# Performance work log

Measured on AMD Instinct MI355X. Metric: run time of the kernel, lower is better.

## Reference

```python
import jax, jax.numpy as jnp
import numpy as np

N_CELL, N_NET, N_GCELL = 50000, 10000, 20000
E = 100000
D = 32   # hidden_node = hidden_net = hidden_hanna = out_node = out_net
DP = 16  # hidden_pin = hidden_edge feats


def setup_inputs() -> dict:
    key = jax.random.key(0)
    ks = jax.random.split(key, 21)
    f = jax.random.normal
    ri = lambda k, n: jax.random.randint(k, (E,), 0, n, dtype=jnp.int32)
    return {
        'node_feat': f(ks[0], (N_CELL, D), jnp.float32),
        'net_feat': f(ks[1], (N_NET, D), jnp.float32),
        'pin_feat': f(ks[2], (E, DP), jnp.float32),
        'hanna_feat': f(ks[3], (N_GCELL, D), jnp.float32),
        'edge_feat': f(ks[4], (E, DP), jnp.float32),
        'pins_src': ri(ks[5], N_CELL), 'pins_dst': ri(ks[6], N_NET),
        'pinned_src': ri(ks[7], N_NET), 'pinned_dst': ri(ks[8], N_CELL),
        'connect_src': ri(ks[9], N_GCELL), 'connect_dst': ri(ks[10], N_GCELL),
        'pt_src': ri(ks[11], N_CELL), 'pt_dst': ri(ks[12], N_GCELL),
        'pf_src': ri(ks[13], N_GCELL), 'pf_dst': ri(ks[14], N_CELL),
        'W_net': f(ks[15], (D, D)) * 0.1, 'b_net': jnp.zeros((D,), jnp.float32),
        'W_topo': f(ks[16], (DP, D * D)) * 0.1, 'b_topo': jnp.zeros((D * D,), jnp.float32),
        'W_pins': f(ks[17], (D, D)) * 0.1, 'b_pins': jnp.zeros((D,), jnp.float32),
        'W_connect': f(ks[18], (D, D)) * 0.1, 'b_connect': jnp.zeros((D,), jnp.float32),
        'W_pt': f(ks[19], (D, D)) * 0.1, 'b_pt': jnp.zeros((D,), jnp.float32),
        'b_pinned': jnp.zeros((D,), jnp.float32), 'b_pf': jnp.zeros((D,), jnp.float32),
    }


def _deg(idx, n):
    # clamped degree, as DGL clamps to min 1
    return jnp.maximum(jax.ops.segment_sum(jnp.ones_like(idx, jnp.float32), idx, n), 1.0)


def graph_conv(h_src, W, b, src, dst, n_src, n_dst):
    # DGL GraphConv with norm='both': D_out^{-1/2} gather -> sum -> D_in^{-1/2}, then W, b
    feat = (h_src * _deg(src, n_src)[:, None] ** -0.5) @ W
    agg = jax.ops.segment_sum(feat[src], dst, n_dst)
    return agg * _deg(dst, n_dst)[:, None] ** -0.5 + b


def nn_conv(h_src, efeat, W_topo, b_topo, bias, src, dst, n_dst):
    # DGL NNConv (aggregator='mean'): per-edge weight from edge_func, mean over in-edges
    d_in = h_src.shape[1]
    w = (efeat @ W_topo + b_topo).reshape(-1, d_in, bias.shape[0])  # (E, d_in, d_out)
    m = jnp.einsum('ei,eio->eo', h_src[src], w)
    return jax.ops.segment_sum(m, dst, n_dst) / _deg(dst, n_dst)[:, None] + bias


def reference(node_feat, net_feat, pin_feat, hanna_feat, edge_feat,
              pins_src, pins_dst, pinned_src, pinned_dst, connect_src, connect_dst,
              pt_src, pt_dst, pf_src, pf_dst,
              W_net, b_net, W_topo, b_topo, W_pins, b_pins,
              W_connect, b_connect, W_pt, b_pt, b_pinned, b_pf):
    # 'pins': cell -> net (GraphConv)
    h_net = graph_conv(node_feat, W_pins, b_pins, pins_src, pins_dst, N_CELL, N_NET)
    # 'pinned': net -> cell (NNConv) + 'point-from': gcell -> cell (NNConv); agg='sum'
    h_cell = (nn_conv(net_feat, pin_feat, W_topo, b_topo, b_pinned, pinned_src, pinned_dst, N_CELL)
              + nn_conv(hanna_feat, edge_feat, W_topo, b_topo, b_pf, pf_src, pf_dst, N_CELL))
    # 'connect': gcell -> gcell + 'point-to': cell -> gcell (GraphConvs); agg='sum'
    h_gcell = (graph_conv(hanna_feat, W_connect, b_connect, connect_src, connect_dst, N_GCELL, N_GCELL)
               + graph_conv(node_feat, W_pt, b_pt, pt_src, pt_dst, N_CELL, N_GCELL))
    return (h_cell, h_net + net_feat @ W_net + b_net, h_gcell)
```

## Files before the change

### kernel.cpp

```cpp
#include <hip/hip_runtime.h>

typedef unsigned short u16;
typedef unsigned int u32;

#define NC 50000
#define NN 10000
#define NG 20000
#define NE 100000
#define NSCAN 150016
#define NBLK 74


__device__ __forceinline__ float bflo(u32 a) { return __uint_as_float(a << 16); }
__device__ __forceinline__ float bfhi(u32 a) { return __uint_as_float(a & 0xFFFF0000u); }
__device__ __forceinline__ u16 fbf(float f) {
  u32 u = __float_as_uint(f);
  return (u16)((u + 0x7FFFu + ((u >> 16) & 1u)) >> 16);
}

__device__ __forceinline__ float nn_msg(int e, int s, const float* __restrict__ ef,
                                        const u16* __restrict__ T,
                                        const float* __restrict__ C, int o) {
  const float4* efp = reinterpret_cast<const float4*>(ef + (size_t)e * 16);
  float4 ea = efp[0], eb = efp[1], ec = efp[2], ed = efp[3];
  const uint4* tp = reinterpret_cast<const uint4*>(T + (size_t)s * 512 + o * 16);
  uint4 ta = tp[0], tb = tp[1];
  float m = C[(size_t)s * 32 + o];
  m += ea.x * bflo(ta.x) + ea.y * bfhi(ta.x) + ea.z * bflo(ta.y) + ea.w * bfhi(ta.y);
  m += eb.x * bflo(ta.z) + eb.y * bfhi(ta.z) + eb.z * bflo(ta.w) + eb.w * bfhi(ta.w);
  m += ec.x * bflo(tb.x) + ec.y * bfhi(tb.x) + ec.z * bflo(tb.y) + ec.w * bfhi(tb.y);
  m += ed.x * bflo(tb.z) + ed.y * bfhi(tb.z) + ed.z * bflo(tb.w) + ed.w * bfhi(tb.w);
  return m;
}

__global__ __launch_bounds__(512, 2) void k_front(
    const float* __restrict__ feat_net, const float* __restrict__ feat_han,
    const float* __restrict__ W_topo, const float* __restrict__ b_topo,
    u16* __restrict__ T_net, u16* __restrict__ T_han,
    float* __restrict__ C_net, float* __restrict__ C_han,
    const int* __restrict__ pins_src, const int* __restrict__ pins_dst,
    const int* __restrict__ pinned_dst, const int* __restrict__ pf_dst,
    const int* __restrict__ connect_src, const int* __restrict__ connect_dst,
    const int* __restrict__ pt_src, const int* __restrict__ pt_dst,
    int* __restrict__ hist, int* __restrict__ srccnt) {
  int b = blockIdx.x;
  int tid = threadIdx.x;
  if (b < 469) {
    __shared__ float hs[64][32];
    int nd0 = b * 64;
    {
      int idx = tid * 4;
      int nl = idx >> 5, i = idx & 31;
      int ng = nd0 + nl;
      int ngc = min(ng, 29999);
      const float* rp = (ngc < NN) ? feat_net + (size_t)ngc * 32
                                   : feat_han + (size_t)(ngc - NN) * 32;
      *reinterpret_cast<float4*>(&hs[nl][i]) =
          *reinterpret_cast<const float4*>(rp + i);
    }
    int j = tid;
    int p = j & 15, o = j >> 4;
    float w[32];
#pragma unroll
    for (int i = 0; i < 32; i++) w[i] = W_topo[p * 1024 + i * 32 + o];
#pragma unroll
    for (int i = 0; i < 32; i++) {
      asm volatile("" : "+v"(w[i]));
    }
    __syncthreads();
#pragma unroll 2
    for (int n = 0; n < 64; n++) {
      const float4* hp = reinterpret_cast<const float4*>(&hs[n][0]);
      float a = 0.f;
#pragma unroll
      for (int q = 0; q < 8; q++) {
        float4 h4 = hp[q];
        a += h4.x * w[4 * q] + h4.y * w[4 * q + 1] +
             h4.z * w[4 * q + 2] + h4.w * w[4 * q + 3];
      }
      int s = nd0 + n;
      if (s < 30000) {
        u16* dst = (s < NN) ? T_net + (size_t)s * 512 + j
                            : T_han + (size_t)(s - NN) * 512 + j;
        *dst = fbf(a);
      }
    }
    return;
  }
  if (b < 2344) {
    int t = (b - 469) * 512 + tid;
    int s2 = t >> 5, o = t & 31;
    bool han = s2 >= NN;
    const float* feat = han ? feat_han : feat_net;
    float* C = han ? C_han : C_net;
    int s = han ? s2 - NN : s2;
    float acc = 0.f;
#pragma unroll 8
    for (int i = 0; i < 32; i++)
      acc += feat[(size_t)s * 32 + i] * b_topo[i * 32 + o];
    C[(size_t)s * 32 + o] = acc;
    return;
  }
  int e = (b - 2344) * 512 + tid;
  if (e >= NE) return;
  atomicAdd(&hist[pins_dst[e]], 1);
  atomicAdd(&hist[10000 + connect_dst[e]], 1);
  atomicAdd(&hist[30000 + pt_dst[e]], 1);
  atomicAdd(&hist[50000 + pinned_dst[e]], 1);
  atomicAdd(&hist[100000 + pf_dst[e]], 1);
  atomicAdd(&srccnt[pins_src[e]], 1);
  atomicAdd(&srccnt[50000 + connect_src[e]], 1);
  atomicAdd(&srccnt[70000 + pt_src[e]], 1);
}

__global__ __launch_bounds__(256) void k_scan1(
    const int* __restrict__ cnt, int* __restrict__ bsum) {
  __shared__ int sm[256];
  int b = blockIdx.x, tid = threadIdx.x;
  int base = b * 2048 + tid * 8;
  int tot = 0;
#pragma unroll
  for (int j = 0; j < 8; j++) {
    int i = base + j;
    tot += (i < NSCAN) ? cnt[i] : 0;
  }
  sm[tid] = tot;
  __syncthreads();
  for (int off = 128; off > 0; off >>= 1) {
    if (tid < off) sm[tid] += sm[tid + off];
    __syncthreads();
  }
  if (tid == 0) bsum[b] = sm[0];
}

__global__ __launch_bounds__(256) void k_scan3(
    const int* __restrict__ cnt, const int* __restrict__ bsum,
    int* __restrict__ bases) {
  __shared__ int sm[256];
  __shared__ int carry;
  int b = blockIdx.x, tid = threadIdx.x;
  if (tid == 0) {
    int run = 0;
    for (int i = 0; i < b; i++) run += bsum[i];
    carry = run;
  }
  int base = b * 2048 + tid * 8;
  int v[8];
  int tot = 0;
#pragma unroll
  for (int j = 0; j < 8; j++) {
    int i = base + j;
    v[j] = (i < NSCAN) ? cnt[i] : 0;
    tot += v[j];
  }
  sm[tid] = tot;
  __syncthreads();
  for (int off = 1; off < 256; off <<= 1) {
    int add = (tid >= off) ? sm[tid - off] : 0;
    __syncthreads();
    sm[tid] += add;
    __syncthreads();
  }
  int excl = sm[tid] - tot + carry;
#pragma unroll
  for (int j = 0; j < 8; j++) {
    int i = base + j;
    if (i < NSCAN) bases[i] = excl;
    excl += v[j];
  }
}

__global__ __launch_bounds__(512) void k_fill(
    const int* __restrict__ pins_src, const int* __restrict__ pins_dst,
    const int* __restrict__ connect_src, const int* __restrict__ connect_dst,
    const int* __restrict__ pt_src, const int* __restrict__ pt_dst,
    const int* __restrict__ pinned_src, const int* __restrict__ pinned_dst,
    const int* __restrict__ pf_src, const int* __restrict__ pf_dst,
    const int* __restrict__ srccnt,
    const int* __restrict__ bases, int* __restrict__ cursor,
    int2* __restrict__ csr_gc, int2* __restrict__ csr_nn) {
  int t = blockIdx.x * 512 + threadIdx.x;
  if (t >= 5 * NE) return;
  int r = (t >= NE) + (t >= 2 * NE) + (t >= 3 * NE) + (t >= 4 * NE);
  int e = t - r * NE;
  const int* srcs = r == 0 ? pins_src : r == 1 ? connect_src
                   : r == 2 ? pt_src : r == 3 ? pinned_src : pf_src;
  const int* dsts = r == 0 ? pins_dst : r == 1 ? connect_dst
                   : r == 2 ? pt_dst : r == 3 ? pinned_dst : pf_dst;
  int off = r == 0 ? 0 : r == 1 ? 10000 : r == 2 ? 30000 : r == 3 ? 50000 : 100000;
  int s = srcs[e];
  int g = off + dsts[e];
  int pos = atomicAdd(&cursor[g], 1);
  int cpos = bases[g] + pos;
  if (r < 3) {
    int soff = r == 0 ? 0 : r == 1 ? 50000 : 70000;
    float w = rsqrtf(fmaxf((float)srccnt[soff + s], 1.f));
    csr_gc[cpos] = make_int2(s, __float_as_int(w));
  } else {
    csr_nn[cpos - 300000] = make_int2(e, s);
  }
}

__global__ __launch_bounds__(512) void k_gc_gather(
    const int* __restrict__ hist, const int* __restrict__ bases,
    const int2* __restrict__ csr_gc,
    const float* __restrict__ node_feat, const float* __restrict__ hanna_feat,
    float* __restrict__ S_net, float* __restrict__ S_conn, float* __restrict__ S_pt) {
  int t = blockIdx.x * 512 + threadIdx.x;
  int rr = t >> 5, o = t & 31;
  int rel = (rr >= 10000) + (rr >= 30000);
  const float* feat = (rel == 1) ? hanna_feat : node_feat;
  float* S = rel == 0 ? S_net + (size_t)rr * 32
           : rel == 1 ? S_conn + (size_t)(rr - 10000) * 32
                      : S_pt + (size_t)(rr - 30000) * 32;
  int base = bases[rr], deg = hist[rr];
  float acc = 0.f;
  int k = 0;
  for (; k + 1 < deg; k += 2) {
    int2 pa = csr_gc[base + k], pb = csr_gc[base + k + 1];
    acc += feat[(size_t)pa.x * 32 + o] * __int_as_float(pa.y) +
           feat[(size_t)pb.x * 32 + o] * __int_as_float(pb.y);
  }
  if (k < deg) {
    int2 pa = csr_gc[base + k];
    acc += feat[(size_t)pa.x * 32 + o] * __int_as_float(pa.y);
  }
  S[o] = acc;
}

__global__ __launch_bounds__(512) void k_tail(
    const int* __restrict__ hist, const int* __restrict__ bases,
    const int2* __restrict__ csr_nn,
    const float* __restrict__ pin_feat, const float* __restrict__ edge_feat,
    const u16* __restrict__ T_net, const u16* __restrict__ T_han,
    const float* __restrict__ C_net, const float* __restrict__ C_han,
    const float* __restrict__ b_pinned, const float* __restrict__ b_pf,
    const float* __restrict__ S_net, const float* __restrict__ net_feat,
    const float* __restrict__ W_pins, const float* __restrict__ b_pins,
    const float* __restrict__ W_net, const float* __restrict__ b_net,
    const float* __restrict__ S_conn, const float* __restrict__ S_pt,
    const float* __restrict__ W_connect, const float* __restrict__ b_connect,
    const float* __restrict__ W_pt, const float* __restrict__ b_pt,
    float* __restrict__ out) {
  __shared__ float Wa[1024], Wb[1024];
  int b = blockIdx.x;
  if (b < 3125) {
    int t = b * 512 + threadIdx.x;
    int d = t >> 5, o = t & 31;
    float a0 = 0.f, a1 = 0.f;
    {
      int g = 50000 + d;
      int base = bases[g] - 300000, deg = hist[g];
      int k = 0;
      for (; k + 1 < deg; k += 2) {
        int2 ea = csr_nn[base + k], eb = csr_nn[base + k + 1];
        a0 += nn_msg(ea.x, ea.y, pin_feat, T_net, C_net, o) +
              nn_msg(eb.x, eb.y, pin_feat, T_net, C_net, o);
      }
      if (k < deg) {
        int2 ea = csr_nn[base + k];
        a0 += nn_msg(ea.x, ea.y, pin_feat, T_net, C_net, o);
      }
      a0 /= fmaxf((float)deg, 1.f);
    }
    {
      int g = 100000 + d;
      int base = bases[g] - 300000, deg = hist[g];
      int k = 0;
      for (; k + 1 < deg; k += 2) {
        int2 ea = csr_nn[base + k], eb = csr_nn[base + k + 1];
        a1 += nn_msg(ea.x, ea.y, edge_feat, T_han, C_han, o) +
              nn_msg(eb.x, eb.y, edge_feat, T_han, C_han, o);
      }
      if (k < deg) {
        int2 ea = csr_nn[base + k];
        a1 += nn_msg(ea.x, ea.y, edge_feat, T_han, C_han, o);
      }
      a1 /= fmaxf((float)deg, 1.f);
    }
    out[(size_t)d * 32 + o] = a0 + a1 + b_pinned[o] + b_pf[o];
    return;
  }
  if (b < 3750) {
    for (int k = threadIdx.x; k < 1024; k += 512) {
      Wa[k] = W_pins[k];
      Wb[k] = W_net[k];
    }
    __syncthreads();
    int t = (b - 3125) * 512 + threadIdx.x;
    int r = t >> 5, o = t & 31;
    float a1 = 0.f, a2 = 0.f;
#pragma unroll 8
    for (int i = 0; i < 32; i++) {
      a1 += S_net[(size_t)r * 32 + i] * Wa[i * 32 + o];
      a2 += net_feat[(size_t)r * 32 + i] * Wb[i * 32 + o];
    }
    out[1600000 + t] = a1 * rsqrtf(fmaxf((float)hist[r], 1.f)) + b_pins[o] +
                       a2 + b_net[o];
    return;
  }
  for (int k = threadIdx.x; k < 1024; k += 512) {
    Wa[k] = W_connect[k];
    Wb[k] = W_pt[k];
  }
  __syncthreads();
  int t = (b - 3750) * 512 + threadIdx.x;
  int r = t >> 5, o = t & 31;
  float a1 = 0.f, a2 = 0.f;
#pragma unroll 8
  for (int i = 0; i < 32; i++) {
    a1 += S_conn[(size_t)r * 32 + i] * Wa[i * 32 + o];
    a2 += S_pt[(size_t)r * 32 + i] * Wb[i * 32 + o];
  }
  out[1920000 + t] = a1 * rsqrtf(fmaxf((float)hist[10000 + r], 1.f)) + b_connect[o] +
                     a2 * rsqrtf(fmaxf((float)hist[30000 + r], 1.f)) + b_pt[o];
}

extern "C" void kernel_launch(void* const* d_in, const int* in_sizes, int n_in,
                              void* d_out, int out_size, void* d_ws, size_t ws_size,
                              hipStream_t stream) {
  const float* node_feat  = (const float*)d_in[0];
  const float* net_feat   = (const float*)d_in[1];
  const float* pin_feat   = (const float*)d_in[2];
  const float* hanna_feat = (const float*)d_in[3];
  const float* edge_feat  = (const float*)d_in[4];
  const int* pins_src    = (const int*)d_in[5];
  const int* pins_dst    = (const int*)d_in[6];
  const int* pinned_src  = (const int*)d_in[7];
  const int* pinned_dst  = (const int*)d_in[8];
  const int* connect_src = (const int*)d_in[9];
  const int* connect_dst = (const int*)d_in[10];
  const int* pt_src      = (const int*)d_in[11];
  const int* pt_dst      = (const int*)d_in[12];
  const int* pf_src      = (const int*)d_in[13];
  const int* pf_dst      = (const int*)d_in[14];
  const float* W_net     = (const float*)d_in[15];
  const float* b_net     = (const float*)d_in[16];
  const float* W_topo    = (const float*)d_in[17];
  const float* b_topo    = (const float*)d_in[18];
  const float* W_pins    = (const float*)d_in[19];
  const float* b_pins    = (const float*)d_in[20];
  const float* W_connect = (const float*)d_in[21];
  const float* b_connect = (const float*)d_in[22];
  const float* W_pt      = (const float*)d_in[23];
  const float* b_pt      = (const float*)d_in[24];
  const float* b_pinned  = (const float*)d_in[25];
  const float* b_pf      = (const float*)d_in[26];
  float* out = (float*)d_out;

  int* wi = (int*)d_ws;
  int* hist    = wi + 0;
  int* cursor  = wi + 150016;
  int* srccnt  = wi + 300032;
  int* bases   = wi + 420032;
  int* bsum    = wi + 570064;
  int2* csr_gc = (int2*)(wi + 570192);
  int2* csr_nn = (int2*)(wi + 1170192);
  float* wf = (float*)d_ws;
  float* S_net  = wf + 1570192;
  float* S_conn = wf + 1890192;
  float* S_pt   = wf + 2530192;
  float* C_net  = wf + 3170192;
  float* C_han  = wf + 3490192;
  u16* T_net = (u16*)((char*)d_ws + 16520832);
  u16* T_han = (u16*)((char*)d_ws + 16520832 + 10240000);

  hipMemsetAsync(d_ws, 0, 420032 * sizeof(int), stream);

  k_front<<<2540, 512, 0, stream>>>(
      net_feat, hanna_feat, W_topo, b_topo, T_net, T_han, C_net, C_han,
      pins_src, pins_dst, pinned_dst, pf_dst, connect_src, connect_dst,
      pt_src, pt_dst, hist, srccnt);

  k_scan1<<<NBLK, 256, 0, stream>>>(hist, bsum);
  k_scan3<<<NBLK, 256, 0, stream>>>(hist, bsum, bases);

  k_fill<<<(5 * NE + 511) / 512, 512, 0, stream>>>(
      pins_src, pins_dst, connect_src, connect_dst, pt_src, pt_dst,
      pinned_src, pinned_dst, pf_src, pf_dst, srccnt, bases, cursor,
      csr_gc, csr_nn);

  k_gc_gather<<<3125, 512, 0, stream>>>(
      hist, bases, csr_gc, node_feat, hanna_feat, S_net, S_conn, S_pt);

  k_tail<<<5000, 512, 0, stream>>>(
      hist, bases, csr_nn, pin_feat, edge_feat,
      T_net, T_han, C_net, C_han, b_pinned, b_pf,
      S_net, net_feat, W_pins, b_pins, W_net, b_net,
      S_conn, S_pt, W_connect, b_connect, W_pt, b_pt, out);
}
```

Before: 288.2 us.

## Split T-projection dot product across lanes and schedule histogram blocks first

The per-node W_topo projection in k_front no longer keeps 32 weights per thread in registers. Each thread now holds 8 weights, and the 32-wide dot product is split across 4 lane groups and combined with two xor shuffles. Each thread covers 4 output columns in sequence and writes one node per group of 4. The atomic histogram blocks also move to the front of the grid so they launch first and overlap with the compute blocks. The aim is lower register pressure and higher occupancy, paid for with extra shuffles and redundant LDS reads.

```diff
diff --git a/kernel.cpp b/kernel.cpp
--- a/kernel.cpp
+++ b/kernel.cpp
@@ -45,9 +45,22 @@
     int* __restrict__ hist, int* __restrict__ srccnt) {
   int b = blockIdx.x;
   int tid = threadIdx.x;
-  if (b < 469) {
+  if (b < 196) {
+    int e = b * 512 + tid;
+    if (e >= NE) return;
+    atomicAdd(&hist[pins_dst[e]], 1);
+    atomicAdd(&hist[10000 + connect_dst[e]], 1);
+    atomicAdd(&hist[30000 + pt_dst[e]], 1);
+    atomicAdd(&hist[50000 + pinned_dst[e]], 1);
+    atomicAdd(&hist[100000 + pf_dst[e]], 1);
+    atomicAdd(&srccnt[pins_src[e]], 1);
+    atomicAdd(&srccnt[50000 + connect_src[e]], 1);
+    atomicAdd(&srccnt[70000 + pt_src[e]], 1);
+    return;
+  }
+  if (b < 665) {
     __shared__ float hs[64][32];
-    int nd0 = b * 64;
+    int nd0 = (b - 196) * 64;
     {
       int idx = tid * 4;
       int nl = idx >> 5, i = idx & 31;
@@ -58,59 +71,52 @@
       *reinterpret_cast<float4*>(&hs[nl][i]) =
           *reinterpret_cast<const float4*>(rp + i);
     }
-    int j = tid;
-    int p = j & 15, o = j >> 4;
-    float w[32];
+    __syncthreads();
+    int l = tid & 63;
+    int wid = tid >> 6;
+    int jj = l & 15;
+    int q = l >> 4;
+#pragma unroll 1
+    for (int g = 0; g < 4; g++) {
+      int j = g * 128 + wid * 16 + jj;
+      int p = j & 15, o = j >> 4;
+      const float* wp = W_topo + p * 1024 + (q * 8) * 32 + o;
+      float w0 = wp[0],   w1 = wp[32],  w2 = wp[64],  w3 = wp[96];
+      float w4 = wp[128], w5 = wp[160], w6 = wp[192], w7 = wp[224];
+      float keep = 0.f;
+      for (int n4 = 0; n4 < 64; n4 += 4) {
 #pragma unroll
-    for (int i = 0; i < 32; i++) w[i] = W_topo[p * 1024 + i * 32 + o];
-#pragma unroll
-    for (int i = 0; i < 32; i++) {
-      asm volatile("" : "+v"(w[i]));
-    }
-    __syncthreads();
-#pragma unroll 2
-    for (int n = 0; n < 64; n++) {
-      const float4* hp = reinterpret_cast<const float4*>(&hs[n][0]);
-      float a = 0.f;
-#pragma unroll
-      for (int q = 0; q < 8; q++) {
-        float4 h4 = hp[q];
-        a += h4.x * w[4 * q] + h4.y * w[4 * q + 1] +
-             h4.z * w[4 * q + 2] + h4.w * w[4 * q + 3];
-      }
-      int s = nd0 + n;
-      if (s < 30000) {
-        u16* dst = (s < NN) ? T_net + (size_t)s * 512 + j
-                            : T_han + (size_t)(s - NN) * 512 + j;
-        *dst = fbf(a);
+        for (int dn = 0; dn < 4; dn++) {
+          const float4* hrow =
+              reinterpret_cast<const float4*>(&hs[n4 + dn][q * 8]);
+          float4 ha = hrow[0], hb = hrow[1];
+          float part = ha.x * w0 + ha.y * w1 + ha.z * w2 + ha.w * w3 +
+                       hb.x * w4 + hb.y * w5 + hb.z * w6 + hb.w * w7;
+          part += __shfl_xor(part, 16);
+          part += __shfl_xor(part, 32);
+          if (dn == q) keep = part;
+        }
+        int s = nd0 + n4 + q;
+        if (s < 30000) {
+          u16* dst = (s < NN) ? T_net + (size_t)s * 512 + j
+                              : T_han + (size_t)(s - NN) * 512 + j;
+          *dst = fbf(keep);
+        }
       }
     }
     return;
   }
-  if (b < 2344) {
-    int t = (b - 469) * 512 + tid;
-    int s2 = t >> 5, o = t & 31;
-    bool han = s2 >= NN;
-    const float* feat = han ? feat_han : feat_net;
-    float* C = han ? C_han : C_net;
-    int s = han ? s2 - NN : s2;
-    float acc = 0.f;
+  int t = (b - 665) * 512 + tid;
+  int s2 = t >> 5, o = t & 31;
+  bool han = s2 >= NN;
+  const float* feat = han ? feat_han : feat_net;
+  float* C = han ? C_han : C_net;
+  int s = han ? s2 - NN : s2;
+  float acc = 0.f;
 #pragma unroll 8
-    for (int i = 0; i < 32; i++)
-      acc += feat[(size_t)s * 32 + i] * b_topo[i * 32 + o];
-    C[(size_t)s * 32 + o] = acc;
-    return;
-  }
-  int e = (b - 2344) * 512 + tid;
-  if (e >= NE) return;
-  atomicAdd(&hist[pins_dst[e]], 1);
-  atomicAdd(&hist[10000 + connect_dst[e]], 1);
-  atomicAdd(&hist[30000 + pt_dst[e]], 1);
-  atomicAdd(&hist[50000 + pinned_dst[e]], 1);
-  atomicAdd(&hist[100000 + pf_dst[e]], 1);
-  atomicAdd(&srccnt[pins_src[e]], 1);
-  atomicAdd(&srccnt[50000 + connect_src[e]], 1);
-  atomicAdd(&srccnt[70000 + pt_src[e]], 1);
+  for (int i = 0; i < 32; i++)
+    acc += feat[(size_t)s * 32 + i] * b_topo[i * 32 + o];
+  C[(size_t)s * 32 + o] = acc;
 }
 
 __global__ __launch_bounds__(256) void k_scan1(
```

After: 304.2 us. 1.06x slower.

## Compute per-node topology projection with split-bf16 MFMA instead of scalar FMA

Applied to the files above, without the earlier changes.

The front kernel's per-node product of features with the reshaped W_topo (64 nodes by 512 outputs by 32 inputs per block) now runs on MFMA 16x16x32 bf16 instructions. Both operands are split into high and low bf16 halves and three MFMAs are combined to keep close to fp32 accuracy. W_topo is staged into padded shared memory in every block, replacing the per-thread register-resident weights. This adds staging and conversion work per block and writes outputs with a scattered 16-bit store pattern.

```diff
diff --git a/kernel.cpp b/kernel.cpp
--- a/kernel.cpp
+++ b/kernel.cpp
@@ -33,6 +33,12 @@
   return m;
 }
 
+typedef float f32x4 __attribute__((ext_vector_type(4)));
+typedef short bf16x8 __attribute__((ext_vector_type(8)));
+
+#define WPAD 4112
+#define HPAD 528
+
 __global__ __launch_bounds__(512, 2) void k_front(
     const float* __restrict__ feat_net, const float* __restrict__ feat_han,
     const float* __restrict__ W_topo, const float* __restrict__ b_topo,
@@ -46,43 +52,60 @@
   int b = blockIdx.x;
   int tid = threadIdx.x;
   if (b < 469) {
-    __shared__ float hs[64][32];
+    __shared__ __align__(16) short Wh[4 * WPAD], Wl[4 * WPAD];
+    __shared__ __align__(16) short Hh[4 * HPAD], Hl[4 * HPAD];
     int nd0 = b * 64;
+    for (int u = tid; u < 16384; u += 512) {
+      int i = u >> 9, j = u & 511;
+      float wv = W_topo[(j & 15) * 1024 + i * 32 + (j >> 4)];
+      u16 wh = fbf(wv);
+      float res = wv - __uint_as_float((u32)wh << 16);
+      int g = i >> 3, t = i & 7;
+      Wh[g * WPAD + j * 8 + t] = (short)wh;
+      Wl[g * WPAD + j * 8 + t] = (short)fbf(res);
+    }
     {
       int idx = tid * 4;
-      int nl = idx >> 5, i = idx & 31;
-      int ng = nd0 + nl;
-      int ngc = min(ng, 29999);
+      int nl = idx >> 5, i0 = idx & 31;
+      int ngc = min(nd0 + nl, 29999);
       const float* rp = (ngc < NN) ? feat_net + (size_t)ngc * 32
                                    : feat_han + (size_t)(ngc - NN) * 32;
-      *reinterpret_cast<float4*>(&hs[nl][i]) =
-          *reinterpret_cast<const float4*>(rp + i);
-    }
-    int j = tid;
-    int p = j & 15, o = j >> 4;
-    float w[32];
+      float4 h4 = *reinterpret_cast<const float4*>(rp + i0);
+      float hv[4] = {h4.x, h4.y, h4.z, h4.w};
 #pragma unroll
-    for (int i = 0; i < 32; i++) w[i] = W_topo[p * 1024 + i * 32 + o];
+      for (int e = 0; e < 4; e++) {
+        int i = i0 + e;
+        int g = i >> 3, t = i & 7;
+        u16 hh = fbf(hv[e]);
+        float res = hv[e] - __uint_as_float((u32)hh << 16);
+        Hh[g * HPAD + nl * 8 + t] = (short)hh;
+        Hl[g * HPAD + nl * 8 + t] = (short)fbf(res);
+      }
+    }
+    __syncthreads();
+    int l = tid & 63, wid = tid >> 6;
+    int rt = wid & 3, ch = wid >> 2;
+    int g = l >> 4, rr = l & 15;
+    bf16x8 Ah = *(const bf16x8*)&Hh[g * HPAD + (rt * 16 + rr) * 8];
+    bf16x8 Al = *(const bf16x8*)&Hl[g * HPAD + (rt * 16 + rr) * 8];
+    int s0 = nd0 + rt * 16 + g * 4;
+    for (int ct = ch * 16; ct < ch * 16 + 16; ct++) {
+      int c0 = ct * 16;
+      bf16x8 Bh = *(const bf16x8*)&Wh[g * WPAD + (c0 + rr) * 8];
+      bf16x8 Bl = *(const bf16x8*)&Wl[g * WPAD + (c0 + rr) * 8];
+      f32x4 acc = {0.f, 0.f, 0.f, 0.f};
+      acc = __builtin_amdgcn_mfma_f32_16x16x32_bf16(Ah, Bh, acc, 0, 0, 0);
+      acc = __builtin_amdgcn_mfma_f32_16x16x32_bf16(Ah, Bl, acc, 0, 0, 0);
+      acc = __builtin_amdgcn_mfma_f32_16x16x32_bf16(Al, Bh, acc, 0, 0, 0);
+      int j = c0 + rr;
 #pragma unroll
-    for (int i = 0; i < 32; i++) {
-      asm volatile("" : "+v"(w[i]));
-    }
-    __syncthreads();
-#pragma unroll 2
-    for (int n = 0; n < 64; n++) {
-      const float4* hp = reinterpret_cast<const float4*>(&hs[n][0]);
-      float a = 0.f;
-#pragma unroll
-      for (int q = 0; q < 8; q++) {
-        float4 h4 = hp[q];
-        a += h4.x * w[4 * q] + h4.y * w[4 * q + 1] +
-             h4.z * w[4 * q + 2] + h4.w * w[4 * q + 3];
-      }
-      int s = nd0 + n;
-      if (s < 30000) {
-        u16* dst = (s < NN) ? T_net + (size_t)s * 512 + j
-                            : T_han + (size_t)(s - NN) * 512 + j;
-        *dst = fbf(a);
+      for (int reg = 0; reg < 4; reg++) {
+        int s = s0 + reg;
+        if (s < 30000) {
+          u16* dst = (s < NN) ? T_net + (size_t)s * 512 + j
+                              : T_han + (size_t)(s - NN) * 512 + j;
+          *dst = fbf(acc[reg]);
+        }
       }
     }
     return;
```

Result: no change. 289.1 us (+0.3%).
